# Kernel tuning notes

Hardware: AMD Instinct MI355X
Metric: run time of the kernel (lower is better)

Reference implementation:

```python
import jax, jax.numpy as jnp
import numpy as np


def _conv1x1(x, w, b):
    # x: [B,C,H,W], w: [O,C], b: [O]  (1x1 conv == per-pixel matmul)
    return jnp.einsum('bchw,oc->bohw', x, w) + b[None, :, None, None]


def setup_inputs() -> dict:
    key = jax.random.key(0)
    ks = jax.random.split(key, 9)
    B, C, H, W = 4, 64, 64, 64
    Ch = C // 2
    s_in = 1.0 / np.sqrt(C)
    s_h = 1.0 / np.sqrt(Ch)
    return {
        'x': jax.random.normal(ks[0], (B, C, H, W), dtype=jnp.float32),
        'w1': jax.random.normal(ks[1], (Ch, C), dtype=jnp.float32) * s_in,
        'b1': jax.random.normal(ks[2], (Ch,), dtype=jnp.float32) * s_in,
        'w2': jax.random.normal(ks[3], (Ch, C), dtype=jnp.float32) * s_in,
        'b2': jax.random.normal(ks[4], (Ch,), dtype=jnp.float32) * s_in,
        'w3': jax.random.normal(ks[5], (Ch, C), dtype=jnp.float32) * s_in,
        'b3': jax.random.normal(ks[6], (Ch,), dtype=jnp.float32) * s_in,
        'w4': jax.random.normal(ks[7], (C, Ch), dtype=jnp.float32) * s_h,
        'b4': jax.random.normal(ks[8], (C,), dtype=jnp.float32) * s_h,
    }


def reference(x, w1, b1, w2, b2, w3, b3, w4, b4):
    B, C, H, W = x.shape
    N = H * W
    # NOTE: original torch code does .view (raw reshape) with NO permute,
    # so channel/spatial axes get mixed exactly as in the source.
    x1 = _conv1x1(x, w1, b1).reshape(B, N, -1)   # [B, N, C/2] (raw reshape)
    x2 = _conv1x1(x, w2, b2).reshape(B, -1, N)   # [B, C/2, N]
    attn = jnp.matmul(x1, x2)                    # [B, N, N]
    # F.softmax with no dim on a 3D tensor -> legacy implicit dim = 0 (batch)
    attn = jax.nn.softmax(attn, axis=0)
    y = _conv1x1(x, w3, b3).reshape(B, N, -1)    # [B, N, C/2]
    y = jnp.matmul(attn, y)                      # [B, N, C/2]
    y = y.reshape(B, -1, H, W)                   # [B, C/2, H, W]
    return _conv1x1(y, w4, b4)                   # [B, C, H, W]
```

## Files before the change

kernel.cpp:

```cpp
#include <hip/hip_runtime.h>


typedef _Float16 half8 __attribute__((ext_vector_type(8)));
typedef _Float16 half4 __attribute__((ext_vector_type(4)));
typedef float f32x4 __attribute__((ext_vector_type(4)));

#define N_PIX 4096
#define NB    4
#define JS    8
#define LOG2E 1.44269504088896f

__global__ __launch_bounds__(256) void convs_kernel(
    const float* __restrict__ x,
    const float* __restrict__ w1, const float* __restrict__ b1,
    const float* __restrict__ w2, const float* __restrict__ b2,
    const float* __restrict__ w3, const float* __restrict__ b3,
    _Float16* __restrict__ X1h, _Float16* __restrict__ X2f, _Float16* __restrict__ Y3f)
{
    const int t = blockIdx.y;
    const float* __restrict__ w  = (t == 0) ? w1 : ((t == 1) ? w2 : w3);
    const float* __restrict__ bb = (t == 0) ? b1 : ((t == 1) ? b2 : b3);

    __shared__ float sw[8][64];
    __shared__ float sbias[8];
    __shared__ _Float16 sbuf[2048];

    const int tid   = threadIdx.x;
    const int b     = blockIdx.x >> 6;
    const int chunk = (blockIdx.x >> 2) & 15;
    const int og    = blockIdx.x & 3;
    const int o0    = og * 8;
    const int hw    = chunk * 256 + tid;

    for (int e = tid; e < 8 * 64; e += 256)
        sw[e >> 6][e & 63] = w[(o0 + (e >> 6)) * 64 + (e & 63)];
    if (tid < 8) sbias[tid] = bb[o0 + tid];
    __syncthreads();

    float xi[64];
    const float* xb = x + b * 64 * N_PIX + hw;
    #pragma unroll
    for (int c = 0; c < 64; c++) xi[c] = xb[c * N_PIX];

    float acc[8];
    #pragma unroll
    for (int oo = 0; oo < 8; oo++) {
        float a0 = sbias[oo], a1 = 0.f, a2 = 0.f, a3 = 0.f;
        #pragma unroll
        for (int c = 0; c < 64; c += 4) {
            a0 += xi[c + 0] * sw[oo][c + 0];
            a1 += xi[c + 1] * sw[oo][c + 1];
            a2 += xi[c + 2] * sw[oo][c + 2];
            a3 += xi[c + 3] * sw[oo][c + 3];
        }
        acc[oo] = (a0 + a1) + (a2 + a3);
    }

    if (t == 0) {
        #pragma unroll
        for (int oo = 0; oo < 8; oo++)
            X1h[b * 131072 + (o0 + oo) * N_PIX + hw] = (_Float16)(acc[oo] * LOG2E);
    } else if (t == 1) {
        #pragma unroll
        for (int oo = 0; oo < 8; oo++)
            sbuf[tid * 8 + oo] = (_Float16)acc[oo];
        __syncthreads();
        const int m    = tid & 15;
        const int jh   = (tid >> 4) & 1;
        const int jt_l = (tid >> 5) & 7;
        const int jl   = jt_l * 32 + ((m >> 2) * 8) + (m & 3) + jh * 4;
        half8 v = *(half8*)&sbuf[jl * 8];
        *(half8*)&X2f[(((b * 128 + chunk * 8 + jt_l) * 2 + jh) * 64 + og * 16 + m) * 8] = v;
    } else {
        const int c  = tid & 31;
        const int jl = tid >> 5;
        #pragma unroll
        for (int oo = 0; oo < 8; oo++)
            sbuf[(oo * 32 + c) * 8 + jl] = (_Float16)acc[oo];
        __syncthreads();
        const int m  = tid & 15;
        const int ch = (tid >> 4) & 1;
        const int oo = (tid >> 5) & 7;
        half8 v = *(half8*)&sbuf[(oo * 32 + ch * 16 + m) * 8];
        const int jt = (o0 + oo) * 4 + (chunk >> 2);
        *(half8*)&Y3f[(((b * 128 + jt) * 2 + ch) * 64 + (chunk & 3) * 16 + m) * 8] = v;
    }
}

__global__ __launch_bounds__(256) void attn_kernel(
    const _Float16* __restrict__ X1h, const _Float16* __restrict__ X2f,
    const _Float16* __restrict__ Y3f, _Float16* __restrict__ OPh)
{
    __shared__ _Float16 sRedH[4 * 64 * 36];

    const int tid  = threadIdx.x;
    const int wv   = tid >> 6;
    const int lane = tid & 63;
    const int m    = lane & 15;
    const int q    = lane >> 4;
    const int i0   = blockIdx.x * 16;
    const int js   = blockIdx.y;
    const int jt0  = js * 16 + wv * 4;

    half8 bx1[NB];
    #pragma unroll
    for (int b = 0; b < NB; b++)
        bx1[b] = *(const half8*)&X1h[b * 131072 + (i0 + m) * 32 + q * 8];

    f32x4 oaccT[NB][2];
    #pragma unroll
    for (int b = 0; b < NB; b++) {
        oaccT[b][0] = (f32x4){0.f, 0.f, 0.f, 0.f};
        oaccT[b][1] = (f32x4){0.f, 0.f, 0.f, 0.f};
    }

    for (int jt = 0; jt < 4; jt++) {
        const int jg = jt0 + jt;

        half8 ax2[NB][2], ay3[NB][2];
        #pragma unroll
        for (int b = 0; b < NB; b++) {
            #pragma unroll
            for (int jh = 0; jh < 2; jh++)
                ax2[b][jh] = *(const half8*)&X2f[(((b * 128 + jg) * 2 + jh) * 64 + lane) * 8];
            #pragma unroll
            for (int ch = 0; ch < 2; ch++)
                ay3[b][ch] = *(const half8*)&Y3f[(((b * 128 + jg) * 2 + ch) * 64 + lane) * 8];
        }

        f32x4 sT[NB][2];
        #pragma unroll
        for (int b = 0; b < NB; b++)
            #pragma unroll
            for (int jh = 0; jh < 2; jh++)
                sT[b][jh] = __builtin_amdgcn_mfma_f32_16x16x32_f16(
                    ax2[b][jh], bx1[b], (f32x4){0.f, 0.f, 0.f, 0.f}, 0, 0, 0);

        half8 pf[NB];
        #pragma unroll
        for (int jh = 0; jh < 2; jh++)
            #pragma unroll
            for (int r = 0; r < 4; r++) {
                float e0 = exp2f(sT[0][jh][r]);
                float e1 = exp2f(sT[1][jh][r]);
                float e2 = exp2f(sT[2][jh][r]);
                float e3 = exp2f(sT[3][jh][r]);
                float rs = __builtin_amdgcn_rcpf(e0 + e1 + e2 + e3);
                pf[0][jh * 4 + r] = (_Float16)(e0 * rs);
                pf[1][jh * 4 + r] = (_Float16)(e1 * rs);
                pf[2][jh * 4 + r] = (_Float16)(e2 * rs);
                pf[3][jh * 4 + r] = (_Float16)(e3 * rs);
            }

        #pragma unroll
        for (int b = 0; b < NB; b++)
            #pragma unroll
            for (int ch = 0; ch < 2; ch++)
                oaccT[b][ch] = __builtin_amdgcn_mfma_f32_16x16x32_f16(
                    ay3[b][ch], pf[b], oaccT[b][ch], 0, 0, 0);
    }

    #pragma unroll
    for (int b = 0; b < NB; b++)
        #pragma unroll
        for (int ch = 0; ch < 2; ch++) {
            half4 h;
            #pragma unroll
            for (int r = 0; r < 4; r++) h[r] = (_Float16)oaccT[b][ch][r];
            *(half4*)&sRedH[(wv * 64 + lane) * 36 + b * 8 + ch * 4] = h;
        }
    __syncthreads();

    const int bb = tid >> 6;
    const int lp = tid & 63;
    const int mm = lp & 15;
    const int qq = lp >> 4;
    #pragma unroll
    for (int ch = 0; ch < 2; ch++) {
        half4 h0 = *(half4*)&sRedH[(0 * 64 + lp) * 36 + bb * 8 + ch * 4];
        half4 h1 = *(half4*)&sRedH[(1 * 64 + lp) * 36 + bb * 8 + ch * 4];
        half4 h2 = *(half4*)&sRedH[(2 * 64 + lp) * 36 + bb * 8 + ch * 4];
        half4 h3 = *(half4*)&sRedH[(3 * 64 + lp) * 36 + bb * 8 + ch * 4];
        half4 v;
        #pragma unroll
        for (int r = 0; r < 4; r++)
            v[r] = (_Float16)(((float)h0[r] + (float)h1[r]) + ((float)h2[r] + (float)h3[r]));
        *(half4*)&OPh[js * 524288 + (bb * 4096 + i0 + mm) * 32 + ch * 16 + qq * 4] = v;
    }
}

__global__ __launch_bounds__(256) void reduce_kernel(
    const _Float16* __restrict__ OPh, float* __restrict__ O)
{
    const int u = blockIdx.x * 256 + threadIdx.x;
    const int base = u * 8;
    float acc[8] = {};
    #pragma unroll
    for (int p = 0; p < JS; p++) {
        half8 v = *(const half8*)&OPh[p * 524288 + base];
        #pragma unroll
        for (int e = 0; e < 8; e++) acc[e] += (float)v[e];
    }
    *(f32x4*)&O[base]     = (f32x4){acc[0], acc[1], acc[2], acc[3]};
    *(f32x4*)&O[base + 4] = (f32x4){acc[4], acc[5], acc[6], acc[7]};
}

__global__ __launch_bounds__(256) void out_kernel(
    const float* __restrict__ O, const float* __restrict__ w4,
    const float* __restrict__ b4, float* __restrict__ out)
{
    __shared__ float sw[16][32];
    __shared__ float sbias[16];
    const int tid = threadIdx.x;
    const int ob  = blockIdx.y * 16;
    for (int e = tid; e < 16 * 32; e += 256)
        sw[e >> 5][e & 31] = w4[(ob + (e >> 5)) * 32 + (e & 31)];
    if (tid < 16) sbias[tid] = b4[ob + tid];
    __syncthreads();

    const int b   = blockIdx.x >> 6;
    const int hw  = (blockIdx.x & 63) * 64 + (tid & 63);
    const int og  = tid >> 6;

    float y2[32];
    #pragma unroll
    for (int ch = 0; ch < 32; ch++)
        y2[ch] = O[b * 131072 + ch * 4096 + hw];

    float* obp = out + b * 64 * N_PIX + hw;
    #pragma unroll
    for (int oo = 0; oo < 4; oo++) {
        const int ol = og * 4 + oo;
        float a0 = sbias[ol], a1 = 0.f, a2 = 0.f, a3 = 0.f;
        #pragma unroll
        for (int c = 0; c < 32; c += 4) {
            a0 += y2[c + 0] * sw[ol][c + 0];
            a1 += y2[c + 1] * sw[ol][c + 1];
            a2 += y2[c + 2] * sw[ol][c + 2];
            a3 += y2[c + 3] * sw[ol][c + 3];
        }
        obp[(ob + ol) * N_PIX] = (a0 + a1) + (a2 + a3);
    }
}

extern "C" void kernel_launch(void* const* d_in, const int* in_sizes, int n_in,
                              void* d_out, int out_size, void* d_ws, size_t ws_size,
                              hipStream_t stream) {
    const float* x  = (const float*)d_in[0];
    const float* w1 = (const float*)d_in[1];
    const float* b1 = (const float*)d_in[2];
    const float* w2 = (const float*)d_in[3];
    const float* b2 = (const float*)d_in[4];
    const float* w3 = (const float*)d_in[5];
    const float* b3 = (const float*)d_in[6];
    const float* w4 = (const float*)d_in[7];
    const float* b4 = (const float*)d_in[8];

    char* wsb = (char*)d_ws;
    _Float16* X1h = (_Float16*)(wsb);
    _Float16* X2f = (_Float16*)(wsb + (1 << 20));
    _Float16* Y3f = (_Float16*)(wsb + (2 << 20));
    _Float16* OPh = (_Float16*)(wsb + (3 << 20));
    float*    O   = (float*)   (wsb + (11 << 20));
    float*    out = (float*)d_out;

    dim3 g1(256, 3);
    convs_kernel<<<g1, 256, 0, stream>>>(x, w1, b1, w2, b2, w3, b3, X1h, X2f, Y3f);
    dim3 g2(256, JS);
    attn_kernel<<<g2, 256, 0, stream>>>(X1h, X2f, Y3f, OPh);
    reduce_kernel<<<256, 256, 0, stream>>>(OPh, O);
    dim3 g4(256, 4);
    out_kernel<<<g4, 256, 0, stream>>>(O, w4, b4, out);
}
```

Measured before the change: 122.4 us.

## Process two query row tiles per attention block to reuse loaded K/V fragments

Each attention block now handles 32 query rows instead of 16, computing two 16-row tiles per iteration. The X2 and Y3 fragments loaded for each key tile are reused across both, halving their global loads per unit of work, and the grid shrinks to 128 blocks in x. The shared-memory cross-wave reduction runs twice with an extra barrier. Separately, the reduce kernel switches to 4 elements per thread over twice as many blocks. The cost is more accumulator registers and fewer attention blocks, which may lower occupancy or leave CUs idle.

```diff
diff --git a/kernel.cpp b/kernel.cpp
--- a/kernel.cpp
+++ b/kernel.cpp
@@ -98,22 +98,27 @@
     const int lane = tid & 63;
     const int m    = lane & 15;
     const int q    = lane >> 4;
-    const int i0   = blockIdx.x * 16;
+    const int i0   = blockIdx.x * 32;
     const int js   = blockIdx.y;
     const int jt0  = js * 16 + wv * 4;
 
-    half8 bx1[NB];
+    half8 bx1[NB][2];
     #pragma unroll
     for (int b = 0; b < NB; b++)
-        bx1[b] = *(const half8*)&X1h[b * 131072 + (i0 + m) * 32 + q * 8];
-
-    f32x4 oaccT[NB][2];
-    #pragma unroll
-    for (int b = 0; b < NB; b++) {
-        oaccT[b][0] = (f32x4){0.f, 0.f, 0.f, 0.f};
-        oaccT[b][1] = (f32x4){0.f, 0.f, 0.f, 0.f};
-    }
-
+        #pragma unroll
+        for (int il = 0; il < 2; il++)
+            bx1[b][il] = *(const half8*)&X1h[b * 131072 + (i0 + il * 16 + m) * 32 + q * 8];
+
+    f32x4 oaccT[NB][2][2];
+    #pragma unroll
+    for (int b = 0; b < NB; b++)
+        #pragma unroll
+        for (int ch = 0; ch < 2; ch++)
+            #pragma unroll
+            for (int il = 0; il < 2; il++)
+                oaccT[b][ch][il] = (f32x4){0.f, 0.f, 0.f, 0.f};
+
+    #pragma unroll 1
     for (int jt = 0; jt < 4; jt++) {
         const int jg = jt0 + jt;
 
@@ -128,64 +133,69 @@
                 ay3[b][ch] = *(const half8*)&Y3f[(((b * 128 + jg) * 2 + ch) * 64 + lane) * 8];
         }
 
-        f32x4 sT[NB][2];
-        #pragma unroll
-        for (int b = 0; b < NB; b++)
+        #pragma unroll
+        for (int il = 0; il < 2; il++) {
+            f32x4 sT[NB][2];
+            #pragma unroll
+            for (int b = 0; b < NB; b++)
+                #pragma unroll
+                for (int jh = 0; jh < 2; jh++)
+                    sT[b][jh] = __builtin_amdgcn_mfma_f32_16x16x32_f16(
+                        ax2[b][jh], bx1[b][il], (f32x4){0.f, 0.f, 0.f, 0.f}, 0, 0, 0);
+
+            half8 pf[NB];
             #pragma unroll
             for (int jh = 0; jh < 2; jh++)
-                sT[b][jh] = __builtin_amdgcn_mfma_f32_16x16x32_f16(
-                    ax2[b][jh], bx1[b], (f32x4){0.f, 0.f, 0.f, 0.f}, 0, 0, 0);
-
-        half8 pf[NB];
-        #pragma unroll
-        for (int jh = 0; jh < 2; jh++)
-            #pragma unroll
-            for (int r = 0; r < 4; r++) {
-                float e0 = exp2f(sT[0][jh][r]);
-                float e1 = exp2f(sT[1][jh][r]);
-                float e2 = exp2f(sT[2][jh][r]);
-                float e3 = exp2f(sT[3][jh][r]);
-                float rs = __builtin_amdgcn_rcpf(e0 + e1 + e2 + e3);
-                pf[0][jh * 4 + r] = (_Float16)(e0 * rs);
-                pf[1][jh * 4 + r] = (_Float16)(e1 * rs);
-                pf[2][jh * 4 + r] = (_Float16)(e2 * rs);
-                pf[3][jh * 4 + r] = (_Float16)(e3 * rs);
-            }
-
-        #pragma unroll
-        for (int b = 0; b < NB; b++)
-            #pragma unroll
-            for (int ch = 0; ch < 2; ch++)
-                oaccT[b][ch] = __builtin_amdgcn_mfma_f32_16x16x32_f16(
-                    ay3[b][ch], pf[b], oaccT[b][ch], 0, 0, 0);
-    }
-
-    #pragma unroll
-    for (int b = 0; b < NB; b++)
-        #pragma unroll
-        for (int ch = 0; ch < 2; ch++) {
-            half4 h;
-            #pragma unroll
-            for (int r = 0; r < 4; r++) h[r] = (_Float16)oaccT[b][ch][r];
-            *(half4*)&sRedH[(wv * 64 + lane) * 36 + b * 8 + ch * 4] = h;
-        }
-    __syncthreads();
+                #pragma unroll
+                for (int r = 0; r < 4; r++) {
+                    float e0 = exp2f(sT[0][jh][r]);
+                    float e1 = exp2f(sT[1][jh][r]);
+                    float e2 = exp2f(sT[2][jh][r]);
+                    float e3 = exp2f(sT[3][jh][r]);
+                    float rs = __builtin_amdgcn_rcpf(e0 + e1 + e2 + e3);
+                    pf[0][jh * 4 + r] = (_Float16)(e0 * rs);
+                    pf[1][jh * 4 + r] = (_Float16)(e1 * rs);
+                    pf[2][jh * 4 + r] = (_Float16)(e2 * rs);
+                    pf[3][jh * 4 + r] = (_Float16)(e3 * rs);
+                }
+
+            #pragma unroll
+            for (int b = 0; b < NB; b++)
+                #pragma unroll
+                for (int ch = 0; ch < 2; ch++)
+                    oaccT[b][ch][il] = __builtin_amdgcn_mfma_f32_16x16x32_f16(
+                        ay3[b][ch], pf[b], oaccT[b][ch][il], 0, 0, 0);
+        }
+    }
 
     const int bb = tid >> 6;
     const int lp = tid & 63;
     const int mm = lp & 15;
     const int qq = lp >> 4;
-    #pragma unroll
-    for (int ch = 0; ch < 2; ch++) {
-        half4 h0 = *(half4*)&sRedH[(0 * 64 + lp) * 36 + bb * 8 + ch * 4];
-        half4 h1 = *(half4*)&sRedH[(1 * 64 + lp) * 36 + bb * 8 + ch * 4];
-        half4 h2 = *(half4*)&sRedH[(2 * 64 + lp) * 36 + bb * 8 + ch * 4];
-        half4 h3 = *(half4*)&sRedH[(3 * 64 + lp) * 36 + bb * 8 + ch * 4];
-        half4 v;
-        #pragma unroll
-        for (int r = 0; r < 4; r++)
-            v[r] = (_Float16)(((float)h0[r] + (float)h1[r]) + ((float)h2[r] + (float)h3[r]));
-        *(half4*)&OPh[js * 524288 + (bb * 4096 + i0 + mm) * 32 + ch * 16 + qq * 4] = v;
+    for (int il = 0; il < 2; il++) {
+        if (il) __syncthreads();
+        #pragma unroll
+        for (int b = 0; b < NB; b++)
+            #pragma unroll
+            for (int ch = 0; ch < 2; ch++) {
+                half4 h;
+                #pragma unroll
+                for (int r = 0; r < 4; r++) h[r] = (_Float16)oaccT[b][ch][il][r];
+                *(half4*)&sRedH[(wv * 64 + lane) * 36 + b * 8 + ch * 4] = h;
+            }
+        __syncthreads();
+        #pragma unroll
+        for (int ch = 0; ch < 2; ch++) {
+            half4 h0 = *(half4*)&sRedH[(0 * 64 + lp) * 36 + bb * 8 + ch * 4];
+            half4 h1 = *(half4*)&sRedH[(1 * 64 + lp) * 36 + bb * 8 + ch * 4];
+            half4 h2 = *(half4*)&sRedH[(2 * 64 + lp) * 36 + bb * 8 + ch * 4];
+            half4 h3 = *(half4*)&sRedH[(3 * 64 + lp) * 36 + bb * 8 + ch * 4];
+            half4 v;
+            #pragma unroll
+            for (int r = 0; r < 4; r++)
+                v[r] = (_Float16)(((float)h0[r] + (float)h1[r]) + ((float)h2[r] + (float)h3[r]));
+            *(half4*)&OPh[js * 524288 + (bb * 4096 + i0 + il * 16 + mm) * 32 + ch * 16 + qq * 4] = v;
+        }
     }
 }
 
@@ -193,16 +203,15 @@
     const _Float16* __restrict__ OPh, float* __restrict__ O)
 {
     const int u = blockIdx.x * 256 + threadIdx.x;
-    const int base = u * 8;
-    float acc[8] = {};
+    const int base = u * 4;
+    float acc[4] = {};
     #pragma unroll
     for (int p = 0; p < JS; p++) {
-        half8 v = *(const half8*)&OPh[p * 524288 + base];
-        #pragma unroll
-        for (int e = 0; e < 8; e++) acc[e] += (float)v[e];
-    }
-    *(f32x4*)&O[base]     = (f32x4){acc[0], acc[1], acc[2], acc[3]};
-    *(f32x4*)&O[base + 4] = (f32x4){acc[4], acc[5], acc[6], acc[7]};
+        half4 v = *(const half4*)&OPh[p * 524288 + base];
+        #pragma unroll
+        for (int e = 0; e < 4; e++) acc[e] += (float)v[e];
+    }
+    *(f32x4*)&O[base] = (f32x4){acc[0], acc[1], acc[2], acc[3]};
 }
 
 __global__ __launch_bounds__(256) void out_kernel(
@@ -266,9 +275,9 @@
 
     dim3 g1(256, 3);
     convs_kernel<<<g1, 256, 0, stream>>>(x, w1, b1, w2, b2, w3, b3, X1h, X2f, Y3f);
-    dim3 g2(256, JS);
+    dim3 g2(128, JS);
     attn_kernel<<<g2, 256, 0, stream>>>(X1h, X2f, Y3f, OPh);
-    reduce_kernel<<<256, 256, 0, stream>>>(OPh, O);
+    reduce_kernel<<<512, 256, 0, stream>>>(OPh, O);
     dim3 g4(256, 4);
     out_kernel<<<g4, 256, 0, stream>>>(O, w4, b4, out);
 }
```

After: 132.3 us. 1.08x slower.

## Split attention over more j-slices and fuse partial reduction into output conv

Applied to the files above, without the earlier changes.

Raises the number of j-splits from 8 to 32 so each attention wave handles one j tile with no inner loop. This adds parallelism and lowers per-wave latency. The separate reduce and out-projection kernels are merged into one kernel that sums the fp16 partials into shared memory and applies the 1x1 conv, which removes a launch and the fp32 intermediate round trip. The cost is four times more partial-output traffic: 32 slices of about 1 MB each written, then read back. That workspace now runs from offset 3 MB to 35 MB.

```diff
diff --git a/kernel.cpp b/kernel.cpp
--- a/kernel.cpp
+++ b/kernel.cpp
@@ -7,7 +7,7 @@
 
 #define N_PIX 4096
 #define NB    4
-#define JS    8
+#define JS    32
 #define LOG2E 1.44269504088896f
 
 __global__ __launch_bounds__(256) void convs_kernel(
@@ -100,65 +100,55 @@
     const int q    = lane >> 4;
     const int i0   = blockIdx.x * 16;
     const int js   = blockIdx.y;
-    const int jt0  = js * 16 + wv * 4;
+    const int jg   = js * 4 + wv;
 
     half8 bx1[NB];
     #pragma unroll
     for (int b = 0; b < NB; b++)
         bx1[b] = *(const half8*)&X1h[b * 131072 + (i0 + m) * 32 + q * 8];
 
+    half8 ax2[NB][2], ay3[NB][2];
+    #pragma unroll
+    for (int b = 0; b < NB; b++) {
+        #pragma unroll
+        for (int jh = 0; jh < 2; jh++)
+            ax2[b][jh] = *(const half8*)&X2f[(((b * 128 + jg) * 2 + jh) * 64 + lane) * 8];
+        #pragma unroll
+        for (int ch = 0; ch < 2; ch++)
+            ay3[b][ch] = *(const half8*)&Y3f[(((b * 128 + jg) * 2 + ch) * 64 + lane) * 8];
+    }
+
+    f32x4 sT[NB][2];
+    #pragma unroll
+    for (int b = 0; b < NB; b++)
+        #pragma unroll
+        for (int jh = 0; jh < 2; jh++)
+            sT[b][jh] = __builtin_amdgcn_mfma_f32_16x16x32_f16(
+                ax2[b][jh], bx1[b], (f32x4){0.f, 0.f, 0.f, 0.f}, 0, 0, 0);
+
+    half8 pf[NB];
+    #pragma unroll
+    for (int jh = 0; jh < 2; jh++)
+        #pragma unroll
+        for (int r = 0; r < 4; r++) {
+            float e0 = exp2f(sT[0][jh][r]);
+            float e1 = exp2f(sT[1][jh][r]);
+            float e2 = exp2f(sT[2][jh][r]);
+            float e3 = exp2f(sT[3][jh][r]);
+            float rs = __builtin_amdgcn_rcpf(e0 + e1 + e2 + e3);
+            pf[0][jh * 4 + r] = (_Float16)(e0 * rs);
+            pf[1][jh * 4 + r] = (_Float16)(e1 * rs);
+            pf[2][jh * 4 + r] = (_Float16)(e2 * rs);
+            pf[3][jh * 4 + r] = (_Float16)(e3 * rs);
+        }
+
     f32x4 oaccT[NB][2];
     #pragma unroll
-    for (int b = 0; b < NB; b++) {
-        oaccT[b][0] = (f32x4){0.f, 0.f, 0.f, 0.f};
-        oaccT[b][1] = (f32x4){0.f, 0.f, 0.f, 0.f};
-    }
-
-    for (int jt = 0; jt < 4; jt++) {
-        const int jg = jt0 + jt;
-
-        half8 ax2[NB][2], ay3[NB][2];
-        #pragma unroll
-        for (int b = 0; b < NB; b++) {
-            #pragma unroll
-            for (int jh = 0; jh < 2; jh++)
-                ax2[b][jh] = *(const half8*)&X2f[(((b * 128 + jg) * 2 + jh) * 64 + lane) * 8];
-            #pragma unroll
-            for (int ch = 0; ch < 2; ch++)
-                ay3[b][ch] = *(const half8*)&Y3f[(((b * 128 + jg) * 2 + ch) * 64 + lane) * 8];
-        }
-
-        f32x4 sT[NB][2];
-        #pragma unroll
-        for (int b = 0; b < NB; b++)
-            #pragma unroll
-            for (int jh = 0; jh < 2; jh++)
-                sT[b][jh] = __builtin_amdgcn_mfma_f32_16x16x32_f16(
-                    ax2[b][jh], bx1[b], (f32x4){0.f, 0.f, 0.f, 0.f}, 0, 0, 0);
-
-        half8 pf[NB];
-        #pragma unroll
-        for (int jh = 0; jh < 2; jh++)
-            #pragma unroll
-            for (int r = 0; r < 4; r++) {
-                float e0 = exp2f(sT[0][jh][r]);
-                float e1 = exp2f(sT[1][jh][r]);
-                float e2 = exp2f(sT[2][jh][r]);
-                float e3 = exp2f(sT[3][jh][r]);
-                float rs = __builtin_amdgcn_rcpf(e0 + e1 + e2 + e3);
-                pf[0][jh * 4 + r] = (_Float16)(e0 * rs);
-                pf[1][jh * 4 + r] = (_Float16)(e1 * rs);
-                pf[2][jh * 4 + r] = (_Float16)(e2 * rs);
-                pf[3][jh * 4 + r] = (_Float16)(e3 * rs);
-            }
-
-        #pragma unroll
-        for (int b = 0; b < NB; b++)
-            #pragma unroll
-            for (int ch = 0; ch < 2; ch++)
-                oaccT[b][ch] = __builtin_amdgcn_mfma_f32_16x16x32_f16(
-                    ay3[b][ch], pf[b], oaccT[b][ch], 0, 0, 0);
-    }
+    for (int b = 0; b < NB; b++)
+        #pragma unroll
+        for (int ch = 0; ch < 2; ch++)
+            oaccT[b][ch] = __builtin_amdgcn_mfma_f32_16x16x32_f16(
+                ay3[b][ch], pf[b], (f32x4){0.f, 0.f, 0.f, 0.f}, 0, 0, 0);
 
     #pragma unroll
     for (int b = 0; b < NB; b++)
@@ -189,57 +179,57 @@
     }
 }
 
-__global__ __launch_bounds__(256) void reduce_kernel(
-    const _Float16* __restrict__ OPh, float* __restrict__ O)
-{
-    const int u = blockIdx.x * 256 + threadIdx.x;
-    const int base = u * 8;
-    float acc[8] = {};
-    #pragma unroll
-    for (int p = 0; p < JS; p++) {
-        half8 v = *(const half8*)&OPh[p * 524288 + base];
-        #pragma unroll
-        for (int e = 0; e < 8; e++) acc[e] += (float)v[e];
-    }
-    *(f32x4*)&O[base]     = (f32x4){acc[0], acc[1], acc[2], acc[3]};
-    *(f32x4*)&O[base + 4] = (f32x4){acc[4], acc[5], acc[6], acc[7]};
-}
-
-__global__ __launch_bounds__(256) void out_kernel(
-    const float* __restrict__ O, const float* __restrict__ w4,
+__global__ __launch_bounds__(256) void reduce_out_kernel(
+    const _Float16* __restrict__ OPh, const float* __restrict__ w4,
     const float* __restrict__ b4, float* __restrict__ out)
 {
-    __shared__ float sw[16][32];
-    __shared__ float sbias[16];
+    __shared__ float sY[32 * 72];
+    __shared__ float sw[64 * 32];
+    __shared__ float sbias[64];
+
     const int tid = threadIdx.x;
-    const int ob  = blockIdx.y * 16;
-    for (int e = tid; e < 16 * 32; e += 256)
-        sw[e >> 5][e & 31] = w4[(ob + (e >> 5)) * 32 + (e & 31)];
-    if (tid < 16) sbias[tid] = b4[ob + tid];
+    for (int e = tid; e < 64 * 32; e += 256) sw[e] = w4[e];
+    if (tid < 64) sbias[tid] = b4[tid];
+
+    const int b   = blockIdx.x >> 6;
+    const int hw0 = (blockIdx.x & 63) * 64;
+
+    const int ch    = tid >> 3;
+    const int piece = tid & 7;
+    {
+        float acc[8] = {};
+        const _Float16* base = OPh + b * 131072 + ch * 4096 + hw0 + piece * 8;
+        #pragma unroll
+        for (int p = 0; p < JS; p++) {
+            half8 v = *(const half8*)&base[p * 524288];
+            #pragma unroll
+            for (int e = 0; e < 8; e++) acc[e] += (float)v[e];
+        }
+        *(f32x4*)&sY[ch * 72 + piece * 8]     = (f32x4){acc[0], acc[1], acc[2], acc[3]};
+        *(f32x4*)&sY[ch * 72 + piece * 8 + 4] = (f32x4){acc[4], acc[5], acc[6], acc[7]};
+    }
     __syncthreads();
 
-    const int b   = blockIdx.x >> 6;
-    const int hw  = (blockIdx.x & 63) * 64 + (tid & 63);
-    const int og  = tid >> 6;
+    const int hw_l = tid & 63;
+    const int og   = tid >> 6;
 
     float y2[32];
     #pragma unroll
-    for (int ch = 0; ch < 32; ch++)
-        y2[ch] = O[b * 131072 + ch * 4096 + hw];
-
-    float* obp = out + b * 64 * N_PIX + hw;
-    #pragma unroll
-    for (int oo = 0; oo < 4; oo++) {
-        const int ol = og * 4 + oo;
-        float a0 = sbias[ol], a1 = 0.f, a2 = 0.f, a3 = 0.f;
+    for (int c = 0; c < 32; c++) y2[c] = sY[c * 72 + hw_l];
+
+    float* obp = out + b * 64 * N_PIX + hw0 + hw_l;
+    #pragma unroll
+    for (int oo = 0; oo < 16; oo++) {
+        const int o = og * 16 + oo;
+        float a0 = sbias[o], a1 = 0.f, a2 = 0.f, a3 = 0.f;
         #pragma unroll
         for (int c = 0; c < 32; c += 4) {
-            a0 += y2[c + 0] * sw[ol][c + 0];
-            a1 += y2[c + 1] * sw[ol][c + 1];
-            a2 += y2[c + 2] * sw[ol][c + 2];
-            a3 += y2[c + 3] * sw[ol][c + 3];
-        }
-        obp[(ob + ol) * N_PIX] = (a0 + a1) + (a2 + a3);
+            a0 += y2[c + 0] * sw[o * 32 + c + 0];
+            a1 += y2[c + 1] * sw[o * 32 + c + 1];
+            a2 += y2[c + 2] * sw[o * 32 + c + 2];
+            a3 += y2[c + 3] * sw[o * 32 + c + 3];
+        }
+        obp[o * N_PIX] = (a0 + a1) + (a2 + a3);
     }
 }
 
@@ -261,14 +251,11 @@
     _Float16* X2f = (_Float16*)(wsb + (1 << 20));
     _Float16* Y3f = (_Float16*)(wsb + (2 << 20));
     _Float16* OPh = (_Float16*)(wsb + (3 << 20));
-    float*    O   = (float*)   (wsb + (11 << 20));
     float*    out = (float*)d_out;
 
     dim3 g1(256, 3);
     convs_kernel<<<g1, 256, 0, stream>>>(x, w1, b1, w2, b2, w3, b3, X1h, X2f, Y3f);
     dim3 g2(256, JS);
     attn_kernel<<<g2, 256, 0, stream>>>(X1h, X2f, Y3f, OPh);
-    reduce_kernel<<<256, 256, 0, stream>>>(OPh, O);
-    dim3 g4(256, 4);
-    out_kernel<<<g4, 256, 0, stream>>>(O, w4, b4, out);
-}
+    reduce_out_kernel<<<256, 256, 0, stream>>>(OPh, w4, b4, out);
+}
```

Result: slower. 130.0 us (+6.2%).
